# Performance work log

Hardware: AMD Instinct MI355X
Metric: run time of the kernel (lower is better)

## Reference

```python
import jax, jax.numpy as jnp
import numpy as np

BN_EPS = 1e-5
MIN_DIST = 1e-10


def _conv_bn_relu(x, w, b, gamma, beta):
    # pointwise Conv1d (kernel=1) == per-point linear, then BatchNorm1d (training-mode
    # batch stats, biased variance, as torch does for normalization), then ReLU.
    y = jnp.einsum('oc,bcn->bon', w, x) + b[None, :, None]
    mu = y.mean(axis=(0, 2))
    var = y.var(axis=(0, 2))
    yn = (y - mu[None, :, None]) * jax.lax.rsqrt(var + BN_EPS)[None, :, None]
    return jax.nn.relu(yn * gamma[None, :, None] + beta[None, :, None])


def setup_inputs() -> dict:
    key = jax.random.key(0)
    ks = jax.random.split(key, 12)
    B, N1, N2, C1, C2 = 8, 8192, 2048, 128, 256
    in_ch = C1 + C2  # 384
    mlp = [256, 128]
    inp = {
        'xyz1': jax.random.normal(ks[0], (B, N1, 3), jnp.float32),
        'xyz2': jax.random.normal(ks[1], (B, N2, 3), jnp.float32),
        'points1': jax.random.normal(ks[2], (B, C1, N1), jnp.float32),
        'points2': jax.random.normal(ks[3], (B, C2, N2), jnp.float32),
    }
    last = in_ch
    for i, out_ch in enumerate(mlp):
        scale = 1.0 / np.sqrt(last)
        inp[f'w{i}'] = jax.random.uniform(ks[4 + 2 * i], (out_ch, last), jnp.float32, -scale, scale)
        inp[f'b{i}'] = jax.random.uniform(ks[5 + 2 * i], (out_ch,), jnp.float32, -scale, scale)
        inp[f'gamma{i}'] = jnp.ones((out_ch,), jnp.float32)
        inp[f'beta{i}'] = jnp.zeros((out_ch,), jnp.float32)
        last = out_ch
    return inp


def reference(xyz1, xyz2, points1, points2,
              w0, b0, gamma0, beta0, w1, b1, gamma1, beta1):
    # Euclidean distance matrix [B, N1, N2] (torch.cdist, p=2)
    sq = (jnp.sum(xyz1 * xyz1, -1)[:, :, None]
          + jnp.sum(xyz2 * xyz2, -1)[:, None, :]
          - 2.0 * jnp.einsum('bnd,bmd->bnm', xyz1, xyz2))
    dists = jnp.sqrt(jnp.maximum(sq, 0.0))
    # 3 smallest distances + indices (ascending, matching torch.topk largest=False)
    neg_d, knn_idx = jax.lax.top_k(-dists, 3)  # [B, N1, 3]
    knn_d = jnp.maximum(-neg_d, MIN_DIST)
    weights = 1.0 / knn_d
    weights = weights / jnp.sum(weights, axis=2, keepdims=True)  # [B, N1, 3]
    # gather neighbor features: points2 [B, C2, N2] -> [B, C2, N1, 3]
    knn_feats = jnp.take_along_axis(points2[:, :, None, :],
                                    knn_idx[:, None, :, :], axis=3)
    interpolated = jnp.sum(knn_feats * weights[:, None, :, :], axis=3)  # [B, C2, N1]
    new_points = jnp.concatenate([points1, interpolated], axis=1)  # [B, C1+C2, N1]
    new_points = _conv_bn_relu(new_points, w0, b0, gamma0, beta0)
    new_points = _conv_bn_relu(new_points, w1, b1, gamma1, beta1)
    return new_points
```

## Files before the change

kernel.cpp:

```cpp
#include <hip/hip_runtime.h>
#include <cstdint>

using u16 = unsigned short;
typedef short bf16x8 __attribute__((ext_vector_type(8)));
typedef float f32x4 __attribute__((ext_vector_type(4)));

__device__ __forceinline__ float bf2f(u16 h) {
    union { unsigned u; float f; } x;
    x.u = ((unsigned)h) << 16;
    return x.f;
}
__device__ __forceinline__ u16 f2bf(float f) {
    union { float f; unsigned u; } x;
    x.f = f;
    unsigned r = x.u + 0x7fffu + ((x.u >> 16) & 1u);
    return (u16)(r >> 16);
}

#define N1 8192
#define N2 2048
#define C2 256

__global__ __launch_bounds__(256) void prep_misc(const float* __restrict__ w0,
                                                 const float* __restrict__ w1,
                                                 const float* __restrict__ xyz2,
                                                 u16* __restrict__ w0b,
                                                 u16* __restrict__ w1b,
                                                 float4* __restrict__ P2P,
                                                 float* __restrict__ stats) {
    int bid = blockIdx.x, tid = threadIdx.x;
    if (bid < 384) {
        int i = bid * 256 + tid;
        w0b[i] = f2bf(w0[i]);
    } else if (bid < 512) {
        int i = (bid - 384) * 256 + tid;
        w1b[i] = f2bf(w1[i]);
    } else if (bid < 576) {
        int i = (bid - 512) * 256 + tid;
        float x = xyz2[i * 3 + 0], y = xyz2[i * 3 + 1], z = xyz2[i * 3 + 2];
        float nsq = __fadd_rn(__fadd_rn(__fmul_rn(x, x), __fmul_rn(y, y)), __fmul_rn(z, z));
        P2P[i] = make_float4(-2.0f * x, -2.0f * y, -2.0f * z, nsq);
    } else {
        for (int i = tid; i < 768; i += 256) stats[i] = 0.0f;
    }
}

__global__ __launch_bounds__(256) void transpose_to_bf16(const float* __restrict__ src,
                                                         u16* __restrict__ dst,
                                                         int C, int N, int dst_stride,
                                                         int col_off) {
    __shared__ float tile[32][33];
    int b = blockIdx.z;
    int n0 = blockIdx.x * 32, c0 = blockIdx.y * 32;
    int tx = threadIdx.x & 31, ty = threadIdx.x >> 5;
    const float* s = src + (long)b * C * N;
#pragma unroll
    for (int i = 0; i < 4; i++) {
        int c = ty + i * 8;
        tile[c][tx] = s[(long)(c0 + c) * N + n0 + tx];
    }
    __syncthreads();
    u16* d = dst + (long)b * N * dst_stride;
#pragma unroll
    for (int i = 0; i < 4; i++) {
        int n = ty + i * 8;
        d[(long)(n0 + n) * dst_stride + col_off + c0 + tx] = f2bf(tile[tx][n]);
    }
}

__global__ __launch_bounds__(512) void knn_interp(const float* __restrict__ xyz1,
                                                  const float4* __restrict__ P2P,
                                                  const u16* __restrict__ P2T,
                                                  u16* __restrict__ X) {
    __shared__ float m_d[8][64][3];
    __shared__ int   m_i[8][64][3];
    __shared__ int   s_idx[64][3];
    __shared__ float s_w[64][3];
    int b = blockIdx.y;
    int n0 = blockIdx.x * 64;
    int tid = threadIdx.x;
    int ql = tid & 63;
    int part = __builtin_amdgcn_readfirstlane(tid >> 6);

    int n = n0 + ql;
    float px = xyz1[((long)b * N1 + n) * 3 + 0];
    float py = xyz1[((long)b * N1 + n) * 3 + 1];
    float pz = xyz1[((long)b * N1 + n) * 3 + 2];
    float psq = __fadd_rn(__fadd_rn(__fmul_rn(px, px), __fmul_rn(py, py)), __fmul_rn(pz, pz));

    const float4* __restrict__ pp = P2P + (long)b * N2 + part * (N2 / 8);
    int jbeg = part * (N2 / 8);
    float b0 = 1e30f, b1 = 1e30f, b2 = 1e30f;
    int i0 = 0, i1 = 0, i2 = 0;
#pragma unroll 4
    for (int jj = 0; jj < N2 / 8; jj++) {
        float4 p = pp[jj];
        float u = __fadd_rn(__fadd_rn(__fmul_rn(p.x, px), __fmul_rn(p.y, py)),
                            __fmul_rn(p.z, pz));
        float sq = __fadd_rn(__fadd_rn(psq, p.w), u);
        int j = jbeg + jj;
        bool c0 = sq < b0, c1 = sq < b1, c2 = sq < b2;
        float t1 = c0 ? b0 : sq;  int ti1 = c0 ? i0 : j;
        b0 = c0 ? sq : b0;        i0 = c0 ? j : i0;
        float t2 = c1 ? b1 : t1;  int ti2 = c1 ? i1 : ti1;
        b1 = c1 ? t1 : b1;        i1 = c1 ? ti1 : i1;
        b2 = c2 ? t2 : b2;        i2 = c2 ? ti2 : i2;
    }
    m_d[part][ql][0] = b0; m_d[part][ql][1] = b1; m_d[part][ql][2] = b2;
    m_i[part][ql][0] = i0; m_i[part][ql][1] = i1; m_i[part][ql][2] = i2;
    __syncthreads();

    if (tid < 64) {
        float c0 = 1e30f, c1 = 1e30f, c2 = 1e30f;
        int a0 = 0x7fffffff, a1 = 0x7fffffff, a2 = 0x7fffffff;
#pragma unroll
        for (int pp2 = 0; pp2 < 8; pp2++) {
#pragma unroll
            for (int k = 0; k < 3; k++) {
                float d = m_d[pp2][tid][k];
                int ix = m_i[pp2][tid][k];
                if (d < c2 || (d == c2 && ix < a2)) {
                    if (d < c1 || (d == c1 && ix < a1)) {
                        c2 = c1; a2 = a1;
                        if (d < c0 || (d == c0 && ix < a0)) { c1 = c0; a1 = a0; c0 = d; a0 = ix; }
                        else                                { c1 = d; a1 = ix; }
                    } else { c2 = d; a2 = ix; }
                }
            }
        }
        float e0 = sqrtf(fmaxf(c0, 0.0f));
        float e1 = sqrtf(fmaxf(c1, 0.0f));
        float e2 = sqrtf(fmaxf(c2, 0.0f));
        float kd0 = fmaxf(e0, 1e-10f), kd1 = fmaxf(e1, 1e-10f), kd2 = fmaxf(e2, 1e-10f);
        float w0 = __fdiv_rn(1.0f, kd0), w1 = __fdiv_rn(1.0f, kd1), w2 = __fdiv_rn(1.0f, kd2);
        float wsum = __fadd_rn(__fadd_rn(w0, w1), w2);
        s_idx[tid][0] = a0; s_idx[tid][1] = a1; s_idx[tid][2] = a2;
        s_w[tid][0] = __fdiv_rn(w0, wsum);
        s_w[tid][1] = __fdiv_rn(w1, wsum);
        s_w[tid][2] = __fdiv_rn(w2, wsum);
    }
    __syncthreads();

    int l = tid & 63;
    const u16* base = P2T + (long)b * N2 * C2;
    for (int p = part; p < 64; p += 8) {
        int j0 = s_idx[p][0], j1 = s_idx[p][1], j2 = s_idx[p][2];
        float f0 = s_w[p][0], f1 = s_w[p][1], f2 = s_w[p][2];
        ushort4 r0 = *(const ushort4*)&base[(long)j0 * C2 + l * 4];
        ushort4 r1 = *(const ushort4*)&base[(long)j1 * C2 + l * 4];
        ushort4 r2 = *(const ushort4*)&base[(long)j2 * C2 + l * 4];
        ushort4 o;
        o.x = f2bf(__fadd_rn(__fadd_rn(__fmul_rn(bf2f(r0.x), f0), __fmul_rn(bf2f(r1.x), f1)),
                             __fmul_rn(bf2f(r2.x), f2)));
        o.y = f2bf(__fadd_rn(__fadd_rn(__fmul_rn(bf2f(r0.y), f0), __fmul_rn(bf2f(r1.y), f1)),
                             __fmul_rn(bf2f(r2.y), f2)));
        o.z = f2bf(__fadd_rn(__fadd_rn(__fmul_rn(bf2f(r0.z), f0), __fmul_rn(bf2f(r1.z), f1)),
                             __fmul_rn(bf2f(r2.z), f2)));
        o.w = f2bf(__fadd_rn(__fadd_rn(__fmul_rn(bf2f(r0.w), f0), __fmul_rn(bf2f(r1.w), f1)),
                             __fmul_rn(bf2f(r2.w), f2)));
        *(ushort4*)&X[(long)(b * N1 + n0 + p) * 384 + 128 + l * 4] = o;
    }
}

template <int KDIM, bool BN_IN, bool OUT_BF16>
__global__ __launch_bounds__(256) void gemm_bn(const u16* __restrict__ A,
                                               const u16* __restrict__ Bw,
                                               const float* __restrict__ bias,
                                               const float* __restrict__ g_in_sum,
                                               const float* __restrict__ g_in_ssq,
                                               const float* __restrict__ gamma_in,
                                               const float* __restrict__ beta_in,
                                               void* __restrict__ Yout, int Ntot,
                                               float* __restrict__ g_out_sum,
                                               float* __restrict__ g_out_ssq) {
    __shared__ __align__(16) u16 Al[128 * 40];
    __shared__ __align__(16) u16 Bl[128 * 40];
    __shared__ float s_stats[256];
    __shared__ float s_scale[BN_IN ? KDIM : 2];
    __shared__ float s_shift[BN_IN ? KDIM : 2];

    int tid = threadIdx.x;
    long s0 = (long)blockIdx.x * 128;
    int o0 = blockIdx.y * 128;

    s_stats[tid < 256 ? tid : 0] = 0.0f;
    if constexpr (BN_IN) {
        for (int k = tid; k < KDIM; k += 256) {
            float mu = g_in_sum[k] * (1.0f / 65536.0f);
            float var = g_in_ssq[k] * (1.0f / 65536.0f) - mu * mu;
            float rs = rsqrtf(var + 1e-5f);
            float sc = gamma_in[k] * rs;
            s_scale[k] = sc;
            s_shift[k] = beta_in[k] - mu * sc;
        }
    }
    int wid = tid >> 6, lane = tid & 63;
    int wm = wid >> 1, wn = wid & 1;
    int q = lane >> 4, l16 = lane & 15;

    f32x4 acc[4][4];
#pragma unroll
    for (int mi = 0; mi < 4; mi++)
#pragma unroll
        for (int ni = 0; ni < 4; ni++) acc[mi][ni] = (f32x4){0.f, 0.f, 0.f, 0.f};
    __syncthreads();

    for (int kt = 0; kt < KDIM; kt += 32) {
#pragma unroll
        for (int cc = 0; cc < 2; cc++) {
            int ci = tid + cc * 256;
            int row = ci >> 2;
            int kc = (ci & 3) << 3;
            union { uint4 u; u16 h[8]; } va;
            va.u = *(const uint4*)(A + (s0 + row) * KDIM + kt + kc);
            if constexpr (BN_IN) {
#pragma unroll
                for (int j = 0; j < 8; j++) {
                    float f = bf2f(va.h[j]);
                    f = fmaxf(fmaf(f, s_scale[kt + kc + j], s_shift[kt + kc + j]), 0.0f);
                    va.h[j] = f2bf(f);
                }
            }
            *(uint4*)&Al[row * 40 + kc] = va.u;
            *(uint4*)&Bl[row * 40 + kc] = *(const uint4*)(Bw + (long)(o0 + row) * KDIM + kt + kc);
        }
        __syncthreads();
        bf16x8 af[4], bfr[4];
#pragma unroll
        for (int mi = 0; mi < 4; mi++)
            af[mi] = *(const bf16x8*)&Al[(wm * 64 + mi * 16 + l16) * 40 + q * 8];
#pragma unroll
        for (int ni = 0; ni < 4; ni++)
            bfr[ni] = *(const bf16x8*)&Bl[(wn * 64 + ni * 16 + l16) * 40 + q * 8];
#pragma unroll
        for (int mi = 0; mi < 4; mi++)
#pragma unroll
            for (int ni = 0; ni < 4; ni++)
                acc[mi][ni] = __builtin_amdgcn_mfma_f32_16x16x32_bf16(af[mi], bfr[ni],
                                                                      acc[mi][ni], 0, 0, 0);
        __syncthreads();
    }

#pragma unroll
    for (int ni = 0; ni < 4; ni++) {
        int coll = wn * 64 + ni * 16 + l16;
        int col = o0 + coll;
        float bz = bias[col];
        float s1 = 0.0f, s2 = 0.0f;
#pragma unroll
        for (int mi = 0; mi < 4; mi++) {
#pragma unroll
            for (int r = 0; r < 4; r++) {
                float v = acc[mi][ni][r] + bz;
                s1 += v;
                s2 += v * v;
                long row = s0 + wm * 64 + mi * 16 + q * 4 + r;
                if constexpr (OUT_BF16)
                    ((u16*)Yout)[row * Ntot + col] = f2bf(v);
                else
                    ((float*)Yout)[row * Ntot + col] = v;
            }
        }
        s1 += __shfl_xor(s1, 16, 64);
        s1 += __shfl_xor(s1, 32, 64);
        s2 += __shfl_xor(s2, 16, 64);
        s2 += __shfl_xor(s2, 32, 64);
        if (q == 0) {
            atomicAdd(&s_stats[coll], s1);
            atomicAdd(&s_stats[128 + coll], s2);
        }
    }
    __syncthreads();
    if (tid < 128) {
        atomicAdd(&g_out_sum[o0 + tid], s_stats[tid]);
        atomicAdd(&g_out_ssq[o0 + tid], s_stats[128 + tid]);
    }
}

__global__ __launch_bounds__(256) void finalize_k(const u16* __restrict__ Y1,
                                                  const float* __restrict__ g_sum,
                                                  const float* __restrict__ g_ssq,
                                                  const float* __restrict__ gamma,
                                                  const float* __restrict__ beta,
                                                  float* __restrict__ out) {
    __shared__ float s_scale[128], s_shift[128];
    int tid = threadIdx.x;
    if (tid < 128) {
        float mu = g_sum[tid] * (1.0f / 65536.0f);
        float var = g_ssq[tid] * (1.0f / 65536.0f) - mu * mu;
        float rs = rsqrtf(var + 1e-5f);
        float sc = gamma[tid] * rs;
        s_scale[tid] = sc;
        s_shift[tid] = beta[tid] - mu * sc;
    }
    __syncthreads();
    long s = (long)blockIdx.x * 256 + tid;
    int b = (int)(s >> 13);
    int n = (int)(s & 8191);
    const u16* yrow = Y1 + s * 128;
    float* obase = out + (long)b * 128 * 8192 + n;
#pragma unroll
    for (int oc = 0; oc < 128; oc += 8) {
        union { uint4 u; u16 h[8]; } va;
        va.u = *(const uint4*)&yrow[oc];
#pragma unroll
        for (int k = 0; k < 8; k++) {
            int o = oc + k;
            float v = fmaxf(fmaf(bf2f(va.h[k]), s_scale[o], s_shift[o]), 0.0f);
            obase[(long)o * 8192] = v;
        }
    }
}

extern "C" void kernel_launch(void* const* d_in, const int* in_sizes, int n_in,
                              void* d_out, int out_size, void* d_ws, size_t ws_size,
                              hipStream_t stream) {
    const float* xyz1    = (const float*)d_in[0];
    const float* xyz2    = (const float*)d_in[1];
    const float* points1 = (const float*)d_in[2];
    const float* points2 = (const float*)d_in[3];
    const float* w0 = (const float*)d_in[4];
    const float* b0 = (const float*)d_in[5];
    const float* gamma0 = (const float*)d_in[6];
    const float* beta0 = (const float*)d_in[7];
    const float* w1 = (const float*)d_in[8];
    const float* b1 = (const float*)d_in[9];
    const float* gamma1 = (const float*)d_in[10];
    const float* beta1 = (const float*)d_in[11];
    float* out = (float*)d_out;

    char* ws = (char*)d_ws;
    u16* X      = (u16*)(ws + 0);
    u16* P2T    = (u16*)(ws + 50331648);
    u16* w0b    = (u16*)(ws + 58720256);
    u16* w1b    = (u16*)(ws + 58916864);
    u16* Y0     = (u16*)(ws + 58982400);
    float4* P2P = (float4*)(ws + 92536832);
    u16* Y1b    = (u16*)(ws + 92798976);
    float* stats = (float*)(ws + 126091264);
    if (ws_size < 126094336) return;
    float* gsum0 = stats;
    float* gss0  = stats + 256;
    float* gsum1 = stats + 512;
    float* gss1  = stats + 640;

    prep_misc<<<577, 256, 0, stream>>>(w0, w1, xyz2, w0b, w1b, P2P, stats);
    transpose_to_bf16<<<dim3(256, 4, 8), 256, 0, stream>>>(points1, X, 128, 8192, 384, 0);
    transpose_to_bf16<<<dim3(64, 8, 8), 256, 0, stream>>>(points2, P2T, 256, 2048, 256, 0);
    knn_interp<<<dim3(128, 8), 512, 0, stream>>>(xyz1, P2P, P2T, X);
    gemm_bn<384, false, true><<<dim3(512, 2), 256, 0, stream>>>(
        X, w0b, b0, nullptr, nullptr, nullptr, nullptr, Y0, 256, gsum0, gss0);
    gemm_bn<256, true, true><<<dim3(512, 1), 256, 0, stream>>>(
        Y0, w1b, b1, gsum0, gss0, gamma0, beta0, Y1b, 128, gsum1, gss1);
    finalize_k<<<256, 256, 0, stream>>>(Y1b, gsum1, gss1, gamma1, beta1, out);
}
```

Baseline: 284.8 us.

## Stage KNN candidates in LDS and use direct global-to-LDS loads in first GEMM

The KNN kernel now copies all xyz2 points for the batch into shared memory once per block and scans them from LDS instead of global memory. Its top-3 insertion uses min/max on the distances with simpler index selects, and the loop unroll goes from 4 to 8. The first GEMM (which has no BN on its input) loads A and B tiles with global_load_lds into an unpadded, XOR-swizzled LDS layout, bypassing registers. The second GEMM keeps the register path. Risks include lower KNN occupancy from the 32KB LDS footprint, and the async loads have no explicit wait before the barrier beyond what the compiler inserts.

Result: faster. 277.6 us (-2.5%).

```diff
diff --git a/kernel.cpp b/kernel.cpp
--- a/kernel.cpp
+++ b/kernel.cpp
@@ -15,6 +15,11 @@
     x.f = f;
     unsigned r = x.u + 0x7fffu + ((x.u >> 16) & 1u);
     return (u16)(r >> 16);
+}
+
+__device__ __forceinline__ void gl_lds16(const u16* g, u16* l) {
+    __builtin_amdgcn_global_load_lds((const __attribute__((address_space(1))) void*)g,
+                                     (__attribute__((address_space(3))) void*)l, 16, 0, 0);
 }
 
 #define N1 8192
@@ -72,6 +77,7 @@
                                                   const float4* __restrict__ P2P,
                                                   const u16* __restrict__ P2T,
                                                   u16* __restrict__ X) {
+    __shared__ float4 pts[N2];
     __shared__ float m_d[8][64][3];
     __shared__ int   m_i[8][64][3];
     __shared__ int   s_idx[64][3];
@@ -82,29 +88,38 @@
     int ql = tid & 63;
     int part = __builtin_amdgcn_readfirstlane(tid >> 6);
 
+    {
+        const float4* src = P2P + (long)b * N2;
+        for (int j = tid; j < N2; j += 512) pts[j] = src[j];
+    }
+
     int n = n0 + ql;
     float px = xyz1[((long)b * N1 + n) * 3 + 0];
     float py = xyz1[((long)b * N1 + n) * 3 + 1];
     float pz = xyz1[((long)b * N1 + n) * 3 + 2];
     float psq = __fadd_rn(__fadd_rn(__fmul_rn(px, px), __fmul_rn(py, py)), __fmul_rn(pz, pz));
-
-    const float4* __restrict__ pp = P2P + (long)b * N2 + part * (N2 / 8);
-    int jbeg = part * (N2 / 8);
+    __syncthreads();
+
+    const float4* lp = &pts[part * (N2 / 8)];
+    int jbase = part * (N2 / 8);
     float b0 = 1e30f, b1 = 1e30f, b2 = 1e30f;
     int i0 = 0, i1 = 0, i2 = 0;
-#pragma unroll 4
+#pragma unroll 8
     for (int jj = 0; jj < N2 / 8; jj++) {
-        float4 p = pp[jj];
+        float4 p = lp[jj];
         float u = __fadd_rn(__fadd_rn(__fmul_rn(p.x, px), __fmul_rn(p.y, py)),
                             __fmul_rn(p.z, pz));
         float sq = __fadd_rn(__fadd_rn(psq, p.w), u);
-        int j = jbeg + jj;
+        int j = jbase + jj;
         bool c0 = sq < b0, c1 = sq < b1, c2 = sq < b2;
-        float t1 = c0 ? b0 : sq;  int ti1 = c0 ? i0 : j;
-        b0 = c0 ? sq : b0;        i0 = c0 ? j : i0;
-        float t2 = c1 ? b1 : t1;  int ti2 = c1 ? i1 : ti1;
-        b1 = c1 ? t1 : b1;        i1 = c1 ? ti1 : i1;
-        b2 = c2 ? t2 : b2;        i2 = c2 ? ti2 : i2;
+        i2 = c2 ? (c1 ? i1 : j) : i2;
+        i1 = c1 ? (c0 ? i0 : j) : i1;
+        i0 = c0 ? j : i0;
+        float m1 = fmaxf(b0, sq);
+        b0 = fminf(b0, sq);
+        float m2 = fmaxf(b1, m1);
+        b1 = fminf(b1, m1);
+        b2 = fminf(b2, m2);
     }
     m_d[part][ql][0] = b0; m_d[part][ql][1] = b1; m_d[part][ql][2] = b2;
     m_i[part][ql][0] = i0; m_i[part][ql][1] = i1; m_i[part][ql][2] = i2;
@@ -162,7 +177,7 @@
     }
 }
 
-template <int KDIM, bool BN_IN, bool OUT_BF16>
+template <int KDIM, bool BN_IN, bool ASYNC>
 __global__ __launch_bounds__(256) void gemm_bn(const u16* __restrict__ A,
                                                const u16* __restrict__ Bw,
                                                const float* __restrict__ bias,
@@ -170,11 +185,12 @@
                                                const float* __restrict__ g_in_ssq,
                                                const float* __restrict__ gamma_in,
                                                const float* __restrict__ beta_in,
-                                               void* __restrict__ Yout, int Ntot,
+                                               u16* __restrict__ Yout, int Ntot,
                                                float* __restrict__ g_out_sum,
                                                float* __restrict__ g_out_ssq) {
-    __shared__ __align__(16) u16 Al[128 * 40];
-    __shared__ __align__(16) u16 Bl[128 * 40];
+    constexpr int LD = ASYNC ? 32 : 40;
+    __shared__ __align__(16) u16 Al[128 * LD];
+    __shared__ __align__(16) u16 Bl[128 * LD];
     __shared__ float s_stats[256];
     __shared__ float s_scale[BN_IN ? KDIM : 2];
     __shared__ float s_shift[BN_IN ? KDIM : 2];
@@ -183,7 +199,7 @@
     long s0 = (long)blockIdx.x * 128;
     int o0 = blockIdx.y * 128;
 
-    s_stats[tid < 256 ? tid : 0] = 0.0f;
+    s_stats[tid] = 0.0f;
     if constexpr (BN_IN) {
         for (int k = tid; k < KDIM; k += 256) {
             float mu = g_in_sum[k] * (1.0f / 65536.0f);
@@ -203,35 +219,56 @@
     for (int mi = 0; mi < 4; mi++)
 #pragma unroll
         for (int ni = 0; ni < 4; ni++) acc[mi][ni] = (f32x4){0.f, 0.f, 0.f, 0.f};
+
+    int rbase0 = wid * 32;
+    int rsub = lane >> 2;
+    int colsw = (((lane & 3) ^ (rsub & 3)) << 3);
+    const u16* gA0 = A + (s0 + rbase0 + rsub) * KDIM + colsw;
+    const u16* gA1 = gA0 + (long)16 * KDIM;
+    const u16* gB0 = Bw + (long)(o0 + rbase0 + rsub) * KDIM + colsw;
+    const u16* gB1 = gB0 + (long)16 * KDIM;
+    u16* lA0 = &Al[rbase0 * 32];
+    u16* lA1 = &Al[(rbase0 + 16) * 32];
+    u16* lB0 = &Bl[rbase0 * 32];
+    u16* lB1 = &Bl[(rbase0 + 16) * 32];
+    int qA = ASYNC ? (q ^ (l16 & 3)) : q;
+
     __syncthreads();
 
     for (int kt = 0; kt < KDIM; kt += 32) {
-#pragma unroll
-        for (int cc = 0; cc < 2; cc++) {
-            int ci = tid + cc * 256;
-            int row = ci >> 2;
-            int kc = (ci & 3) << 3;
-            union { uint4 u; u16 h[8]; } va;
-            va.u = *(const uint4*)(A + (s0 + row) * KDIM + kt + kc);
-            if constexpr (BN_IN) {
-#pragma unroll
-                for (int j = 0; j < 8; j++) {
-                    float f = bf2f(va.h[j]);
-                    f = fmaxf(fmaf(f, s_scale[kt + kc + j], s_shift[kt + kc + j]), 0.0f);
-                    va.h[j] = f2bf(f);
+        if constexpr (ASYNC) {
+            gl_lds16(gA0 + kt, lA0);
+            gl_lds16(gA1 + kt, lA1);
+            gl_lds16(gB0 + kt, lB0);
+            gl_lds16(gB1 + kt, lB1);
+        } else {
+#pragma unroll
+            for (int cc = 0; cc < 2; cc++) {
+                int ci = tid + cc * 256;
+                int row = ci >> 2;
+                int kc = (ci & 3) << 3;
+                union { uint4 u; u16 h[8]; } va;
+                va.u = *(const uint4*)(A + (s0 + row) * KDIM + kt + kc);
+                if constexpr (BN_IN) {
+#pragma unroll
+                    for (int j = 0; j < 8; j++) {
+                        float f = bf2f(va.h[j]);
+                        f = fmaxf(fmaf(f, s_scale[kt + kc + j], s_shift[kt + kc + j]), 0.0f);
+                        va.h[j] = f2bf(f);
+                    }
                 }
+                *(uint4*)&Al[row * LD + kc] = va.u;
+                *(uint4*)&Bl[row * LD + kc] = *(const uint4*)(Bw + (long)(o0 + row) * KDIM + kt + kc);
             }
-            *(uint4*)&Al[row * 40 + kc] = va.u;
-            *(uint4*)&Bl[row * 40 + kc] = *(const uint4*)(Bw + (long)(o0 + row) * KDIM + kt + kc);
         }
         __syncthreads();
         bf16x8 af[4], bfr[4];
 #pragma unroll
         for (int mi = 0; mi < 4; mi++)
-            af[mi] = *(const bf16x8*)&Al[(wm * 64 + mi * 16 + l16) * 40 + q * 8];
+            af[mi] = *(const bf16x8*)&Al[(wm * 64 + mi * 16 + l16) * LD + qA * 8];
 #pragma unroll
         for (int ni = 0; ni < 4; ni++)
-            bfr[ni] = *(const bf16x8*)&Bl[(wn * 64 + ni * 16 + l16) * 40 + q * 8];
+            bfr[ni] = *(const bf16x8*)&Bl[(wn * 64 + ni * 16 + l16) * LD + qA * 8];
 #pragma unroll
         for (int mi = 0; mi < 4; mi++)
 #pragma unroll
@@ -255,10 +292,7 @@
                 s1 += v;
                 s2 += v * v;
                 long row = s0 + wm * 64 + mi * 16 + q * 4 + r;
-                if constexpr (OUT_BF16)
-                    ((u16*)Yout)[row * Ntot + col] = f2bf(v);
-                else
-                    ((float*)Yout)[row * Ntot + col] = v;
+                Yout[row * Ntot + col] = f2bf(v);
             }
         }
         s1 += __shfl_xor(s1, 16, 64);
@@ -350,7 +384,7 @@
     knn_interp<<<dim3(128, 8), 512, 0, stream>>>(xyz1, P2P, P2T, X);
     gemm_bn<384, false, true><<<dim3(512, 2), 256, 0, stream>>>(
         X, w0b, b0, nullptr, nullptr, nullptr, nullptr, Y0, 256, gsum0, gss0);
-    gemm_bn<256, true, true><<<dim3(512, 1), 256, 0, stream>>>(
+    gemm_bn<256, true, false><<<dim3(512, 1), 256, 0, stream>>>(
         Y0, w1b, b1, gsum0, gss0, gamma0, beta0, Y1b, 128, gsum1, gss1);
     finalize_k<<<256, 256, 0, stream>>>(Y1b, gsum1, gss1, gamma1, beta1, out);
 }
```
